# Kernel tuning notes

Measured on AMD Instinct MI355X. Metric: run time of the kernel, lower is better.

Reference implementation:

```python
import jax, jax.numpy as jnp
import numpy as np

B, L, XS, YS, A, C, NL = 32, 4096, 256, 256, 4, 64, 5  # batch, seq, x_size, y_size, n_actions, hid_cnn, cnn_layers


def _conv2d(x, w):
    # x: [N,Cin,H,W], w: [Cout,Cin,3,3], stride 1, pad 1 ('SAME')
    return jax.lax.conv_general_dilated(x, w, (1, 1), 'SAME',
                                        dimension_numbers=('NCHW', 'OIHW', 'NCHW'))


def setup_inputs() -> dict:
    key = jax.random.key(0)
    ks = jax.random.split(key, 16)
    stdv = 1.0 / np.sqrt(XS)
    inp = {
        'x': jax.random.normal(ks[0], (B, L, XS), jnp.float32),
        'y': jax.random.normal(ks[1], (B, YS), jnp.float32),
        'x_mask': jax.random.randint(ks[2], (B, L), 0, 2) == 1,
        'actions': jax.random.randint(ks[3], (B,), 0, A),
        'weight': jax.random.uniform(ks[4], (YS, XS), jnp.float32, -stdv, stdv),
    }
    chans = [(1, C)] + [(C, C)] * (NL - 2) + [(C, 1)]
    for i, (ci, co) in enumerate(chans):
        bound = 1.0 / np.sqrt(ci * 9)
        inp[f'cw{i}'] = jax.random.uniform(ks[5 + 2 * i], (A, co, ci, 3, 3), jnp.float32, -bound, bound)
        inp[f'cb{i}'] = jax.random.uniform(ks[6 + 2 * i], (A, co), jnp.float32, -bound, bound)
    return inp


def reference(x, y, x_mask, actions, weight,
              cw0, cb0, cw1, cb1, cw2, cb2, cw3, cb3, cw4, cb4):
    img = weight[None, None]  # [1,1,YS,XS] -- weight matrix as a 1-channel image

    def per_action(w0, b0, w1, b1, w2, b2, w3, b3, w4, b4):
        out = img
        layers = ((w0, b0), (w1, b1), (w2, b2), (w3, b3), (w4, b4))
        for i, (w, b) in enumerate(layers):
            out = _conv2d(out, w) + b[None, :, None, None]
            if i < NL - 1:
                out = jax.nn.relu(out)
        return out[0, 0]  # [YS,XS]

    # all per-action conv stacks batched via vmap -> [A,YS,XS]
    W_a = jax.vmap(per_action)(cw0, cb0, cw1, cb1, cw2, cb2, cw3, cb3, cw4, cb4)
    # one-hot multiply + sum over actions == select the per-sample action matrix
    Wy = jnp.einsum('bh,bhx->bx', y, W_a[actions])          # [B,XS]
    xWy = jnp.einsum('blx,bx->bl', x, Wy)                   # [B,L]
    xWy = jnp.where(x_mask, -jnp.inf, xWy)
    return jax.nn.softmax(xWy, axis=-1)  # eval-mode output (training uses log_softmax)
```

## Files before the change

### kernel.cpp

```cpp
#include <hip/hip_runtime.h>
#include <cstdint>
#include <cstddef>

typedef __attribute__((ext_vector_type(8))) short bf16x8;
typedef __attribute__((ext_vector_type(4))) float f32x4;
typedef __attribute__((ext_vector_type(4))) int i32x4;

__device__ inline unsigned short cvt_bf16_rne(float f) {
    unsigned u = __builtin_bit_cast(unsigned, f);
    u = (u + 0x7FFFu + ((u >> 16) & 1u)) >> 16;
    return (unsigned short)u;
}
__device__ inline float bf16_to_f32(unsigned short s) {
    return __builtin_bit_cast(float, (unsigned)s << 16);
}

__global__ void detect_mask_kernel(const unsigned int* m, int* flag) {
    int i = blockIdx.x * blockDim.x + threadIdx.x;
    int f = 0;
    #pragma unroll
    for (int k = 0; k < 4; ++k) {
        unsigned int v = m[i * 4 + k];
        if (v == 0x3F800000u) f |= 2;
        else if (v > 1u) f |= 1;
    }
    if (f) atomicOr(flag, f);
}

__global__ void apack_all_kernel(const float* __restrict__ cw1,
                                 const float* __restrict__ cw2,
                                 const float* __restrict__ cw3,
                                 char* __restrict__ apack,
                                 int* __restrict__ flag) {
    int t = threadIdx.x;
    int tap = blockIdx.x, a = blockIdx.y, lz = blockIdx.z;
    if (tap == 0 && a == 0 && lz == 0 && t == 0) *flag = 0;
    const float* cw = (lz == 0) ? cw1 : (lz == 1 ? cw2 : cw3);
    char* outp = apack + (size_t)lz * 294912;
    int ks = t >> 8, mf = (t >> 6) & 3, lane = t & 63;
    int n = lane & 15, q = lane >> 4;
    int co = mf * 16 + n;
    int ci0 = ks * 32 + q * 8;
    unsigned d[4];
    #pragma unroll
    for (int jj = 0; jj < 4; ++jj) {
        unsigned short h0 = cvt_bf16_rne(cw[((size_t)(a * 64 + co) * 64 + ci0 + 2 * jj + 0) * 9 + tap]);
        unsigned short h1 = cvt_bf16_rne(cw[((size_t)(a * 64 + co) * 64 + ci0 + 2 * jj + 1) * 9 + tap]);
        d[jj] = (unsigned)h0 | ((unsigned)h1 << 16);
    }
    *(i32x4*)(outp + ((((size_t)(a * 9 + tap) * 2 + ks) * 4 + mf) * 1024 + lane * 16)) =
        *(i32x4*)d;
}

__device__ __forceinline__ void conv_mid_body(const i32x4* lds4,
                                              const char* __restrict__ apack_l,
                                              const float* __restrict__ cb,
                                              unsigned short* __restrict__ act_out,
                                              int a, int r0, int c0, int tid) {
    int lane = tid & 63, wv = tid >> 6;
    int n = lane & 15, q = lane >> 4;

    f32x4 acc[4][4];
    #pragma unroll
    for (int mf = 0; mf < 4; ++mf) {
        f32x4 bb = *(const f32x4*)(cb + a * 64 + mf * 16 + q * 4);
        #pragma unroll
        for (int nf = 0; nf < 4; ++nf) acc[mf][nf] = bb;
    }

    int base_nf[4];
    #pragma unroll
    for (int nf = 0; nf < 4; ++nf) {
        int orl = wv * 2 + (nf >> 1);
        int ocl = ((nf & 1) << 4) + n;
        base_nf[nf] = (orl * 34 + ocl) * 9 + q;
    }
    const char* ap = apack_l + (size_t)a * 9 * 8192 + lane * 16;

    #pragma unroll
    for (int tap = 0; tap < 9; ++tap) {
        const int ty = tap / 3, tx = tap - ty * 3;
        const int toff = (ty * 34 + tx) * 9;
        #pragma unroll
        for (int ks = 0; ks < 2; ++ks) {
            bf16x8 Af[4], Bf[4];
            #pragma unroll
            for (int mf = 0; mf < 4; ++mf)
                Af[mf] = __builtin_bit_cast(bf16x8,
                    *(const i32x4*)(ap + (((tap * 2 + ks) * 4 + mf) << 10)));
            #pragma unroll
            for (int nf = 0; nf < 4; ++nf)
                Bf[nf] = __builtin_bit_cast(bf16x8, lds4[base_nf[nf] + toff + ks * 4]);
            #pragma unroll
            for (int mf = 0; mf < 4; ++mf)
                #pragma unroll
                for (int nf = 0; nf < 4; ++nf)
                    acc[mf][nf] = __builtin_amdgcn_mfma_f32_16x16x32_bf16(
                        Af[mf], Bf[nf], acc[mf][nf], 0, 0, 0);
        }
    }

    #pragma unroll
    for (int nf = 0; nf < 4; ++nf) {
        int grow = r0 + wv * 2 + (nf >> 1);
        int gcol = c0 + ((nf & 1) << 4) + n;
        char* ob = (char*)act_out + (((size_t)(a << 16) + (grow << 8) + gcol) << 7) + q * 8;
        #pragma unroll
        for (int mf = 0; mf < 4; ++mf) {
            f32x4 v = acc[mf][nf];
            unsigned d0 = (unsigned)cvt_bf16_rne(fmaxf(v.x, 0.0f))
                        | ((unsigned)cvt_bf16_rne(fmaxf(v.y, 0.0f)) << 16);
            unsigned d1 = (unsigned)cvt_bf16_rne(fmaxf(v.z, 0.0f))
                        | ((unsigned)cvt_bf16_rne(fmaxf(v.w, 0.0f)) << 16);
            uint2 st; st.x = d0; st.y = d1;
            *(uint2*)(ob + mf * 32) = st;
        }
    }
}

__global__ __launch_bounds__(256, 3)
void conv_mid_mfma(const unsigned short* __restrict__ act_in,
                   const char* __restrict__ apack_l,
                   const float* __restrict__ cb,
                   unsigned short* __restrict__ act_out) {
    __shared__ i32x4 lds4[340 * 9];
    int tid = threadIdx.x;
    int a = blockIdx.z;
    int r0 = blockIdx.y * 8, c0 = blockIdx.x * 32;
    const char* actb = (const char*)act_in;

    for (int s = tid; s < 2720; s += 256) {
        int px = s >> 3, o = s & 7;
        int prow = px / 34, pcol = px - prow * 34;
        int grow = r0 - 1 + prow, gcol = c0 - 1 + pcol;
        i32x4 v = {0, 0, 0, 0};
        if ((unsigned)grow < 256u && (unsigned)gcol < 256u)
            v = *(const i32x4*)(actb + (((size_t)(a << 16) + (grow << 8) + gcol) << 7) + (o << 4));
        lds4[px * 9 + o] = v;
    }
    __syncthreads();
    conv_mid_body(lds4, apack_l, cb, act_out, a, r0, c0, tid);
}

__global__ __launch_bounds__(256, 3)
void conv_mid_fused0(const float* __restrict__ img,
                     const float* __restrict__ cw0,
                     const float* __restrict__ cb0,
                     const char* __restrict__ apack_l,
                     const float* __restrict__ cb,
                     unsigned short* __restrict__ act_out) {
    __shared__ i32x4 lds4[340 * 9];
    __shared__ float img_s[12 * 36];
    int tid = threadIdx.x;
    int a = blockIdx.z;
    int r0 = blockIdx.y * 8, c0 = blockIdx.x * 32;

    for (int s = tid; s < 432; s += 256) {
        int ir = s / 36, ic = s - ir * 36;
        int gr = r0 - 2 + ir, gc = c0 - 2 + ic;
        img_s[s] = ((unsigned)gr < 256u && (unsigned)gc < 256u) ? img[gr * 256 + gc] : 0.0f;
    }
    __syncthreads();

    int o = tid & 7;
    float wr[8][9], br[8];
    #pragma unroll
    for (int j = 0; j < 8; ++j) {
        const float* wp = cw0 + ((size_t)a * 64 + o * 8 + j) * 9;
        #pragma unroll
        for (int t = 0; t < 9; ++t) wr[j][t] = wp[t];
        br[j] = cb0[a * 64 + o * 8 + j];
    }

    for (int s = tid; s < 2720; s += 256) {
        int px = s >> 3;
        int prow = px / 34, pcol = px - prow * 34;
        int grow = r0 - 1 + prow, gcol = c0 - 1 + pcol;
        i32x4 v = {0, 0, 0, 0};
        if ((unsigned)grow < 256u && (unsigned)gcol < 256u) {
            float accv[8];
            #pragma unroll
            for (int j = 0; j < 8; ++j) accv[j] = br[j];
            #pragma unroll
            for (int dy = 0; dy < 3; ++dy)
                #pragma unroll
                for (int dx = 0; dx < 3; ++dx) {
                    float iv = img_s[(prow + dy) * 36 + (pcol + dx)];
                    #pragma unroll
                    for (int j = 0; j < 8; ++j)
                        accv[j] = fmaf(wr[j][dy * 3 + dx], iv, accv[j]);
                }
            unsigned d[4];
            #pragma unroll
            for (int jj = 0; jj < 4; ++jj) {
                unsigned short h0 = cvt_bf16_rne(fmaxf(accv[2 * jj + 0], 0.0f));
                unsigned short h1 = cvt_bf16_rne(fmaxf(accv[2 * jj + 1], 0.0f));
                d[jj] = (unsigned)h0 | ((unsigned)h1 << 16);
            }
            v = *(i32x4*)d;
        }
        lds4[px * 9 + o] = v;
    }
    __syncthreads();
    conv_mid_body(lds4, apack_l, cb, act_out, a, r0, c0, tid);
}

__global__ void conv_last_kernel(const unsigned short* __restrict__ act,
                                 const float* __restrict__ cw4,
                                 const float* __restrict__ cb4,
                                 float* __restrict__ W_a) {
    int y = blockIdx.x, a = blockIdx.y;
    int tid = threadIdx.x;
    int lane = tid & 63, wv = tid >> 6;
    int o = lane & 7, pl = lane >> 3;
    float wr[8][9];
    #pragma unroll
    for (int j = 0; j < 8; ++j) {
        const float* wp = cw4 + ((size_t)a * 64 + o * 8 + j) * 9;
        #pragma unroll
        for (int t = 0; t < 9; ++t) wr[j][t] = wp[t];
    }
    const char* actb = (const char*)act;
    float bias = cb4[a];
    for (int i = 0; i < 8; ++i) {
        int x = i * 32 + wv * 8 + pl;
        float p = 0.0f;
        #pragma unroll
        for (int ty = 0; ty < 3; ++ty) {
            int py = y + ty - 1;
            #pragma unroll
            for (int tx = 0; tx < 3; ++tx) {
                int px = x + tx - 1;
                if ((unsigned)py < 256u && (unsigned)px < 256u) {
                    i32x4 v = *(const i32x4*)(actb +
                        (((size_t)(a << 16) + (py << 8) + px) << 7) + (o << 4));
                    const unsigned* dv = (const unsigned*)&v;
                    #pragma unroll
                    for (int j = 0; j < 8; ++j) {
                        unsigned d = dv[j >> 1];
                        unsigned short us = (j & 1) ? (unsigned short)(d >> 16)
                                                    : (unsigned short)(d & 0xffffu);
                        p = fmaf(bf16_to_f32(us), wr[j][ty * 3 + tx], p);
                    }
                }
            }
        }
        p += __shfl_xor(p, 1, 64);
        p += __shfl_xor(p, 2, 64);
        p += __shfl_xor(p, 4, 64);
        if (o == 0) W_a[(size_t)(a << 16) + (y << 8) + x] = p + bias;
    }
}

__global__ void wy_kernel(const float* __restrict__ yv,
                          const int* __restrict__ actions,
                          const float* __restrict__ W_a,
                          float* __restrict__ Wy) {
    int b = blockIdx.x, t = threadIdx.x;
    int x = t >> 2, hq = t & 3;
    int a = actions[b];
    const float* Wp = W_a + (size_t)a * 65536;
    const float* yb = yv + b * 256;
    float acc = 0.0f;
    #pragma unroll 8
    for (int i = 0; i < 64; ++i) {
        int h = i * 4 + hq;
        acc = fmaf(yb[h], Wp[(size_t)h * 256 + x], acc);
    }
    acc += __shfl_xor(acc, 1, 64);
    acc += __shfl_xor(acc, 2, 64);
    if (hq == 0) Wy[b * 256 + x] = acc;
}

__global__ __launch_bounds__(256)
void logits_kernel(const float* __restrict__ xv,
                   const void* __restrict__ mask,
                   const int* __restrict__ flag,
                   const float* __restrict__ Wy,
                   float* __restrict__ out) {
    int tid = threadIdx.x, lane = tid & 63, w = tid >> 6;
    int i = lane & 15, r = lane >> 4;
    int b = blockIdx.y;
    int fl = *flag;
    float4 wyv[4];
    #pragma unroll
    for (int k = 0; k < 4; ++k)
        wyv[k] = *(const float4*)(Wy + b * 256 + k * 64 + i * 4);
    const float* xb = xv + (size_t)b * 4096 * 256;
    float ninf = -__builtin_inff();
    int base0 = blockIdx.x * 64 + w * 16;

    #pragma unroll 1
    for (int it = 0; it < 4; ++it) {
        int row = base0 + it * 4 + r;
        const float* rp = xb + (size_t)row * 256 + i * 4;
        float4 xq[4];
        #pragma unroll
        for (int k = 0; k < 4; ++k)
            xq[k] = *(const float4*)(rp + k * 64);
        float p = 0.0f;
        #pragma unroll
        for (int k = 0; k < 4; ++k) {
            p = fmaf(xq[k].x, wyv[k].x, p);
            p = fmaf(xq[k].y, wyv[k].y, p);
            p = fmaf(xq[k].z, wyv[k].z, p);
            p = fmaf(xq[k].w, wyv[k].w, p);
        }
        p += __shfl_xor(p, 8, 64);
        p += __shfl_xor(p, 4, 64);
        p += __shfl_xor(p, 2, 64);
        p += __shfl_xor(p, 1, 64);
        if (i == 0) {
            size_t mi = (size_t)b * 4096 + row;
            bool msk;
            if (fl & 2)      msk = ((const float*)mask)[mi] != 0.0f;
            else if (fl & 1) msk = ((const unsigned char*)mask)[mi] != 0;
            else             msk = ((const int*)mask)[mi] != 0;
            out[mi] = msk ? ninf : p;
        }
    }
}

__global__ void softmax_kernel(float* __restrict__ out) {
    int b = blockIdx.x, tid = threadIdx.x;
    int lane = tid & 63, wid = tid >> 6;
    float* row = out + (size_t)b * 4096;
    float v[4];
    float m = -__builtin_inff();
    #pragma unroll
    for (int i = 0; i < 4; ++i) { v[i] = row[tid + i * 1024]; m = fmaxf(m, v[i]); }
    #pragma unroll
    for (int off = 32; off > 0; off >>= 1) m = fmaxf(m, __shfl_xor(m, off, 64));
    __shared__ float redm[16];
    __shared__ float reds[16];
    if (lane == 0) redm[wid] = m;
    __syncthreads();
    float M = redm[0];
    #pragma unroll
    for (int j = 1; j < 16; ++j) M = fmaxf(M, redm[j]);
    float s = 0.0f;
    #pragma unroll
    for (int i = 0; i < 4; ++i) { v[i] = expf(v[i] - M); s += v[i]; }
    #pragma unroll
    for (int off = 32; off > 0; off >>= 1) s += __shfl_xor(s, off, 64);
    if (lane == 0) reds[wid] = s;
    __syncthreads();
    float S = 0.0f;
    #pragma unroll
    for (int j = 0; j < 16; ++j) S += reds[j];
    float inv = 1.0f / S;
    #pragma unroll
    for (int i = 0; i < 4; ++i) row[tid + i * 1024] = v[i] * inv;
}

extern "C" void kernel_launch(void* const* d_in, const int* in_sizes, int n_in,
                              void* d_out, int out_size, void* d_ws, size_t ws_size,
                              hipStream_t stream) {
    const float* xv      = (const float*)d_in[0];
    const float* yv      = (const float*)d_in[1];
    const void*  xmask   = d_in[2];
    const int*   actions = (const int*)d_in[3];
    const float* weight  = (const float*)d_in[4];
    const float* cw0 = (const float*)d_in[5];
    const float* cb0 = (const float*)d_in[6];
    const float* cw1 = (const float*)d_in[7];
    const float* cb1 = (const float*)d_in[8];
    const float* cw2 = (const float*)d_in[9];
    const float* cb2 = (const float*)d_in[10];
    const float* cw3 = (const float*)d_in[11];
    const float* cb3 = (const float*)d_in[12];
    const float* cw4 = (const float*)d_in[13];
    const float* cb4 = (const float*)d_in[14];
    float* out = (float*)d_out;

    char* ws = (char*)d_ws;
    unsigned short* bufA = (unsigned short*)ws;
    unsigned short* bufB = (unsigned short*)(ws + 33554432);
    char*  apack = ws + 67108864;
    float* W_a   = (float*)(ws + 67993600);
    float* Wy    = (float*)(ws + 69042176);
    int*   flag  = (int*)(ws + 69074944);

    apack_all_kernel<<<dim3(9, 4, 3), 512, 0, stream>>>(cw1, cw2, cw3, apack, flag);
    detect_mask_kernel<<<32, 256, 0, stream>>>((const unsigned int*)xmask, flag);

    conv_mid_fused0<<<dim3(8, 32, 4), 256, 0, stream>>>(weight, cw0, cb0, apack, cb1, bufA);
    conv_mid_mfma<<<dim3(8, 32, 4), 256, 0, stream>>>(bufA, apack + 294912, cb2, bufB);
    conv_mid_mfma<<<dim3(8, 32, 4), 256, 0, stream>>>(bufB, apack + 589824, cb3, bufA);
    conv_last_kernel<<<dim3(256, 4), 256, 0, stream>>>(bufA, cw4, cb4, W_a);

    wy_kernel<<<32, 1024, 0, stream>>>(yv, actions, W_a, Wy);
    logits_kernel<<<dim3(64, 32), 256, 0, stream>>>(xv, xmask, flag, Wy, out);
    softmax_kernel<<<32, 1024, 0, stream>>>(out);
}
```

Measured before the change: 358.4 us.

## Fuse final 64-to-1 conv into layer-3 MFMA kernel via scatter atomics

The last conv layer (64 to 1 channel) now runs in the epilogue of the layer-3 MFMA kernel. Each pixel's ReLU'd, bf16-rounded activations are dotted with all 9 taps of cw4 and scattered into W_a with atomicAdd. This removes the bf16 activation write and reread plus a separate kernel launch. In exchange, W_a must be zeroed in the packing kernel and the cb4 bias is folded into wy_kernel as cb4*sum(y). Float atomic ordering makes the results nondeterministic.

Result: slower. 387.7 us (+8.2%).

```diff
diff --git a/kernel.cpp b/kernel.cpp
--- a/kernel.cpp
+++ b/kernel.cpp
@@ -30,11 +30,21 @@
 __global__ void apack_all_kernel(const float* __restrict__ cw1,
                                  const float* __restrict__ cw2,
                                  const float* __restrict__ cw3,
+                                 const float* __restrict__ cw4,
                                  char* __restrict__ apack,
+                                 float* __restrict__ W_a,
+                                 float* __restrict__ w4pack,
                                  int* __restrict__ flag) {
     int t = threadIdx.x;
     int tap = blockIdx.x, a = blockIdx.y, lz = blockIdx.z;
     if (tap == 0 && a == 0 && lz == 0 && t == 0) *flag = 0;
+
+    int gid = ((lz * 4 + a) * 9 + tap) * 512 + t;
+    for (int i = gid; i < 262144; i += 55296) W_a[i] = 0.0f;
+
+    if (lz == 0 && t < 64)
+        w4pack[(a * 9 + tap) * 64 + t] = cw4[(size_t)a * 576 + t * 9 + tap];
+
     const float* cw = (lz == 0) ? cw1 : (lz == 1 ? cw2 : cw3);
     char* outp = apack + (size_t)lz * 294912;
     int ks = t >> 8, mf = (t >> 6) & 3, lane = t & 63;
@@ -52,15 +62,14 @@
         *(i32x4*)d;
 }
 
-__device__ __forceinline__ void conv_mid_body(const i32x4* lds4,
-                                              const char* __restrict__ apack_l,
-                                              const float* __restrict__ cb,
-                                              unsigned short* __restrict__ act_out,
-                                              int a, int r0, int c0, int tid) {
+__device__ __forceinline__ void conv_mid_mainloop(const i32x4* lds4,
+                                                  const char* __restrict__ apack_l,
+                                                  const float* __restrict__ cb,
+                                                  f32x4 acc[4][4],
+                                                  int a, int tid) {
     int lane = tid & 63, wv = tid >> 6;
     int n = lane & 15, q = lane >> 4;
 
-    f32x4 acc[4][4];
     #pragma unroll
     for (int mf = 0; mf < 4; ++mf) {
         f32x4 bb = *(const f32x4*)(cb + a * 64 + mf * 16 + q * 4);
@@ -99,7 +108,13 @@
                         Af[mf], Bf[nf], acc[mf][nf], 0, 0, 0);
         }
     }
-
+}
+
+__device__ __forceinline__ void conv_mid_store(f32x4 acc[4][4],
+                                               unsigned short* __restrict__ act_out,
+                                               int a, int r0, int c0, int tid) {
+    int lane = tid & 63, wv = tid >> 6;
+    int n = lane & 15, q = lane >> 4;
     #pragma unroll
     for (int nf = 0; nf < 4; ++nf) {
         int grow = r0 + wv * 2 + (nf >> 1);
@@ -115,6 +130,20 @@
             uint2 st; st.x = d0; st.y = d1;
             *(uint2*)(ob + mf * 32) = st;
         }
+    }
+}
+
+__device__ __forceinline__ void conv_mid_stage(i32x4* lds4,
+                                               const char* __restrict__ actb,
+                                               int a, int r0, int c0, int tid) {
+    for (int s = tid; s < 2720; s += 256) {
+        int px = s >> 3, o = s & 7;
+        int prow = px / 34, pcol = px - prow * 34;
+        int grow = r0 - 1 + prow, gcol = c0 - 1 + pcol;
+        i32x4 v = {0, 0, 0, 0};
+        if ((unsigned)grow < 256u && (unsigned)gcol < 256u)
+            v = *(const i32x4*)(actb + (((size_t)(a << 16) + (grow << 8) + gcol) << 7) + (o << 4));
+        lds4[px * 9 + o] = v;
     }
 }
 
@@ -127,19 +156,80 @@
     int tid = threadIdx.x;
     int a = blockIdx.z;
     int r0 = blockIdx.y * 8, c0 = blockIdx.x * 32;
-    const char* actb = (const char*)act_in;
-
-    for (int s = tid; s < 2720; s += 256) {
-        int px = s >> 3, o = s & 7;
-        int prow = px / 34, pcol = px - prow * 34;
-        int grow = r0 - 1 + prow, gcol = c0 - 1 + pcol;
-        i32x4 v = {0, 0, 0, 0};
-        if ((unsigned)grow < 256u && (unsigned)gcol < 256u)
-            v = *(const i32x4*)(actb + (((size_t)(a << 16) + (grow << 8) + gcol) << 7) + (o << 4));
-        lds4[px * 9 + o] = v;
-    }
-    __syncthreads();
-    conv_mid_body(lds4, apack_l, cb, act_out, a, r0, c0, tid);
+    conv_mid_stage(lds4, (const char*)act_in, a, r0, c0, tid);
+    __syncthreads();
+    f32x4 acc[4][4];
+    conv_mid_mainloop(lds4, apack_l, cb, acc, a, tid);
+    conv_mid_store(acc, act_out, a, r0, c0, tid);
+}
+
+__global__ __launch_bounds__(256, 3)
+void conv_mid_last_fused(const unsigned short* __restrict__ act_in,
+                         const char* __restrict__ apack_l,
+                         const float* __restrict__ cb,
+                         const float* __restrict__ w4pack,
+                         float* __restrict__ W_a) {
+    __shared__ i32x4 lds4[340 * 9];
+    int tid = threadIdx.x;
+    int a = blockIdx.z;
+    int r0 = blockIdx.y * 8, c0 = blockIdx.x * 32;
+    conv_mid_stage(lds4, (const char*)act_in, a, r0, c0, tid);
+    __syncthreads();
+    f32x4 acc[4][4];
+    conv_mid_mainloop(lds4, apack_l, cb, acc, a, tid);
+
+    int lane = tid & 63, wv = tid >> 6;
+    int n = lane & 15, q = lane >> 4;
+    const float* w4p = w4pack + a * 576;
+
+    float part[4][9];
+    #pragma unroll
+    for (int nf = 0; nf < 4; ++nf)
+        #pragma unroll
+        for (int tap = 0; tap < 9; ++tap) part[nf][tap] = 0.0f;
+
+    #pragma unroll
+    for (int mf = 0; mf < 4; ++mf) {
+        f32x4 wq[9];
+        #pragma unroll
+        for (int tap = 0; tap < 9; ++tap)
+            wq[tap] = *(const f32x4*)(w4p + tap * 64 + mf * 16 + q * 4);
+        #pragma unroll
+        for (int nf = 0; nf < 4; ++nf) {
+            f32x4 v = acc[mf][nf];
+            float a0 = bf16_to_f32(cvt_bf16_rne(fmaxf(v.x, 0.0f)));
+            float a1 = bf16_to_f32(cvt_bf16_rne(fmaxf(v.y, 0.0f)));
+            float a2 = bf16_to_f32(cvt_bf16_rne(fmaxf(v.z, 0.0f)));
+            float a3 = bf16_to_f32(cvt_bf16_rne(fmaxf(v.w, 0.0f)));
+            #pragma unroll
+            for (int tap = 0; tap < 9; ++tap) {
+                float s = part[nf][tap];
+                s = fmaf(a0, wq[tap].x, s);
+                s = fmaf(a1, wq[tap].y, s);
+                s = fmaf(a2, wq[tap].z, s);
+                s = fmaf(a3, wq[tap].w, s);
+                part[nf][tap] = s;
+            }
+        }
+    }
+
+    #pragma unroll
+    for (int nf = 0; nf < 4; ++nf) {
+        int r = r0 + wv * 2 + (nf >> 1);
+        int c = c0 + ((nf & 1) << 4) + n;
+        #pragma unroll
+        for (int tap = 0; tap < 9; ++tap) {
+            float s = part[nf][tap];
+            s += __shfl_xor(s, 16, 64);
+            s += __shfl_xor(s, 32, 64);
+            if (q == 0) {
+                int ty = tap / 3, tx = tap - ty * 3;
+                int yy = r + 1 - ty, xx = c + 1 - tx;
+                if ((unsigned)yy < 256u && (unsigned)xx < 256u)
+                    atomicAdd(W_a + ((size_t)(a << 16) + (yy << 8) + xx), s);
+            }
+        }
+    }
 }
 
 __global__ __launch_bounds__(256, 3)
@@ -202,74 +292,34 @@
         lds4[px * 9 + o] = v;
     }
     __syncthreads();
-    conv_mid_body(lds4, apack_l, cb, act_out, a, r0, c0, tid);
-}
-
-__global__ void conv_last_kernel(const unsigned short* __restrict__ act,
-                                 const float* __restrict__ cw4,
-                                 const float* __restrict__ cb4,
-                                 float* __restrict__ W_a) {
-    int y = blockIdx.x, a = blockIdx.y;
-    int tid = threadIdx.x;
-    int lane = tid & 63, wv = tid >> 6;
-    int o = lane & 7, pl = lane >> 3;
-    float wr[8][9];
-    #pragma unroll
-    for (int j = 0; j < 8; ++j) {
-        const float* wp = cw4 + ((size_t)a * 64 + o * 8 + j) * 9;
-        #pragma unroll
-        for (int t = 0; t < 9; ++t) wr[j][t] = wp[t];
-    }
-    const char* actb = (const char*)act;
-    float bias = cb4[a];
-    for (int i = 0; i < 8; ++i) {
-        int x = i * 32 + wv * 8 + pl;
-        float p = 0.0f;
-        #pragma unroll
-        for (int ty = 0; ty < 3; ++ty) {
-            int py = y + ty - 1;
-            #pragma unroll
-            for (int tx = 0; tx < 3; ++tx) {
-                int px = x + tx - 1;
-                if ((unsigned)py < 256u && (unsigned)px < 256u) {
-                    i32x4 v = *(const i32x4*)(actb +
-                        (((size_t)(a << 16) + (py << 8) + px) << 7) + (o << 4));
-                    const unsigned* dv = (const unsigned*)&v;
-                    #pragma unroll
-                    for (int j = 0; j < 8; ++j) {
-                        unsigned d = dv[j >> 1];
-                        unsigned short us = (j & 1) ? (unsigned short)(d >> 16)
-                                                    : (unsigned short)(d & 0xffffu);
-                        p = fmaf(bf16_to_f32(us), wr[j][ty * 3 + tx], p);
-                    }
-                }
-            }
-        }
-        p += __shfl_xor(p, 1, 64);
-        p += __shfl_xor(p, 2, 64);
-        p += __shfl_xor(p, 4, 64);
-        if (o == 0) W_a[(size_t)(a << 16) + (y << 8) + x] = p + bias;
-    }
+    f32x4 acc[4][4];
+    conv_mid_mainloop(lds4, apack_l, cb, acc, a, tid);
+    conv_mid_store(acc, act_out, a, r0, c0, tid);
 }
 
 __global__ void wy_kernel(const float* __restrict__ yv,
                           const int* __restrict__ actions,
                           const float* __restrict__ W_a,
+                          const float* __restrict__ cb4,
                           float* __restrict__ Wy) {
     int b = blockIdx.x, t = threadIdx.x;
     int x = t >> 2, hq = t & 3;
     int a = actions[b];
     const float* Wp = W_a + (size_t)a * 65536;
     const float* yb = yv + b * 256;
-    float acc = 0.0f;
+    float acc = 0.0f, ys = 0.0f;
     #pragma unroll 8
     for (int i = 0; i < 64; ++i) {
         int h = i * 4 + hq;
-        acc = fmaf(yb[h], Wp[(size_t)h * 256 + x], acc);
+        float yh = yb[h];
+        ys += yh;
+        acc = fmaf(yh, Wp[(size_t)h * 256 + x], acc);
     }
     acc += __shfl_xor(acc, 1, 64);
     acc += __shfl_xor(acc, 2, 64);
-    if (hq == 0) Wy[b * 256 + x] = acc;
+    ys  += __shfl_xor(ys, 1, 64);
+    ys  += __shfl_xor(ys, 2, 64);
+    if (hq == 0) Wy[b * 256 + x] = acc + cb4[a] * ys;
 }
 
 __global__ __launch_bounds__(256)
@@ -376,20 +426,22 @@
     char* ws = (char*)d_ws;
     unsigned short* bufA = (unsigned short*)ws;
     unsigned short* bufB = (unsigned short*)(ws + 33554432);
-    char*  apack = ws + 67108864;
-    float* W_a   = (float*)(ws + 67993600);
-    float* Wy    = (float*)(ws + 69042176);
-    int*   flag  = (int*)(ws + 69074944);
-
-    apack_all_kernel<<<dim3(9, 4, 3), 512, 0, stream>>>(cw1, cw2, cw3, apack, flag);
+    char*  apack  = ws + 67108864;
+    float* W_a    = (float*)(ws + 67993600);
+    float* Wy     = (float*)(ws + 69042176);
+    int*   flag   = (int*)(ws + 69074944);
+    float* w4pack = (float*)(ws + 69075456);
+
+    apack_all_kernel<<<dim3(9, 4, 3), 512, 0, stream>>>(cw1, cw2, cw3, cw4,
+                                                        apack, W_a, w4pack, flag);
     detect_mask_kernel<<<32, 256, 0, stream>>>((const unsigned int*)xmask, flag);
 
     conv_mid_fused0<<<dim3(8, 32, 4), 256, 0, stream>>>(weight, cw0, cb0, apack, cb1, bufA);
     conv_mid_mfma<<<dim3(8, 32, 4), 256, 0, stream>>>(bufA, apack + 294912, cb2, bufB);
-    conv_mid_mfma<<<dim3(8, 32, 4), 256, 0, stream>>>(bufB, apack + 589824, cb3, bufA);
-    conv_last_kernel<<<dim3(256, 4), 256, 0, stream>>>(bufA, cw4, cb4, W_a);
-
-    wy_kernel<<<32, 1024, 0, stream>>>(yv, actions, W_a, Wy);
+    conv_mid_last_fused<<<dim3(8, 32, 4), 256, 0, stream>>>(bufB, apack + 589824, cb3,
+                                                            w4pack, W_a);
+
+    wy_kernel<<<32, 1024, 0, stream>>>(yv, actions, W_a, cb4, Wy);
     logits_kernel<<<dim3(64, 32), 256, 0, stream>>>(xv, xmask, flag, Wy, out);
     softmax_kernel<<<32, 1024, 0, stream>>>(out);
 }
```

## Tile last conv through LDS, fold mask detection into first conv, swizzle XCD

Applied to the files above, without the earlier changes.

The last conv layer is retiled into 8x32 spatial blocks that stage the bf16 activation halo in LDS, replacing per-pixel global loads that re-read each neighbour nine times. The separate mask-detection kernel is merged into the first conv launch as an extra z-slice of blocks, which saves one launch. Block indices are remapped with an XCD swizzle so neighbouring tiles of the same action run on the same chiplet and share L2. The changes add LDS pressure to the last conv kernel and a branch to the fused first kernel.

Result: faster. 341.6 us (-4.7%).

```diff
diff --git a/kernel.cpp b/kernel.cpp
--- a/kernel.cpp
+++ b/kernel.cpp
@@ -15,16 +15,8 @@
     return __builtin_bit_cast(float, (unsigned)s << 16);
 }
 
-__global__ void detect_mask_kernel(const unsigned int* m, int* flag) {
-    int i = blockIdx.x * blockDim.x + threadIdx.x;
-    int f = 0;
-    #pragma unroll
-    for (int k = 0; k < 4; ++k) {
-        unsigned int v = m[i * 4 + k];
-        if (v == 0x3F800000u) f |= 2;
-        else if (v > 1u) f |= 1;
-    }
-    if (f) atomicOr(flag, f);
+__device__ __forceinline__ int xcd_swz1024(int lin) {
+    return (lin & 7) * 128 + (lin >> 3);
 }
 
 __global__ void apack_all_kernel(const float* __restrict__ cw1,
@@ -52,15 +44,14 @@
         *(i32x4*)d;
 }
 
-__device__ __forceinline__ void conv_mid_body(const i32x4* lds4,
-                                              const char* __restrict__ apack_l,
-                                              const float* __restrict__ cb,
-                                              unsigned short* __restrict__ act_out,
-                                              int a, int r0, int c0, int tid) {
+__device__ __forceinline__ void conv_mid_mainloop(const i32x4* lds4,
+                                                  const char* __restrict__ apack_l,
+                                                  const float* __restrict__ cb,
+                                                  f32x4 acc[4][4],
+                                                  int a, int tid) {
     int lane = tid & 63, wv = tid >> 6;
     int n = lane & 15, q = lane >> 4;
 
-    f32x4 acc[4][4];
     #pragma unroll
     for (int mf = 0; mf < 4; ++mf) {
         f32x4 bb = *(const f32x4*)(cb + a * 64 + mf * 16 + q * 4);
@@ -99,7 +90,13 @@
                         Af[mf], Bf[nf], acc[mf][nf], 0, 0, 0);
         }
     }
-
+}
+
+__device__ __forceinline__ void conv_mid_store(f32x4 acc[4][4],
+                                               unsigned short* __restrict__ act_out,
+                                               int a, int r0, int c0, int tid) {
+    int lane = tid & 63, wv = tid >> 6;
+    int n = lane & 15, q = lane >> 4;
     #pragma unroll
     for (int nf = 0; nf < 4; ++nf) {
         int grow = r0 + wv * 2 + (nf >> 1);
@@ -118,17 +115,9 @@
     }
 }
 
-__global__ __launch_bounds__(256, 3)
-void conv_mid_mfma(const unsigned short* __restrict__ act_in,
-                   const char* __restrict__ apack_l,
-                   const float* __restrict__ cb,
-                   unsigned short* __restrict__ act_out) {
-    __shared__ i32x4 lds4[340 * 9];
-    int tid = threadIdx.x;
-    int a = blockIdx.z;
-    int r0 = blockIdx.y * 8, c0 = blockIdx.x * 32;
-    const char* actb = (const char*)act_in;
-
+__device__ __forceinline__ void conv_mid_stage(i32x4* lds4,
+                                               const char* __restrict__ actb,
+                                               int a, int r0, int c0, int tid) {
     for (int s = tid; s < 2720; s += 256) {
         int px = s >> 3, o = s & 7;
         int prow = px / 34, pcol = px - prow * 34;
@@ -138,8 +127,24 @@
             v = *(const i32x4*)(actb + (((size_t)(a << 16) + (grow << 8) + gcol) << 7) + (o << 4));
         lds4[px * 9 + o] = v;
     }
-    __syncthreads();
-    conv_mid_body(lds4, apack_l, cb, act_out, a, r0, c0, tid);
+}
+
+__global__ __launch_bounds__(256, 3)
+void conv_mid_mfma(const unsigned short* __restrict__ act_in,
+                   const char* __restrict__ apack_l,
+                   const float* __restrict__ cb,
+                   unsigned short* __restrict__ act_out) {
+    __shared__ i32x4 lds4[340 * 9];
+    int tid = threadIdx.x;
+    int lin = blockIdx.x + (blockIdx.y << 3) + (blockIdx.z << 8);
+    int wg = xcd_swz1024(lin);
+    int a = wg >> 8;
+    int r0 = ((wg >> 3) & 31) * 8, c0 = (wg & 7) * 32;
+    conv_mid_stage(lds4, (const char*)act_in, a, r0, c0, tid);
+    __syncthreads();
+    f32x4 acc[4][4];
+    conv_mid_mainloop(lds4, apack_l, cb, acc, a, tid);
+    conv_mid_store(acc, act_out, a, r0, c0, tid);
 }
 
 __global__ __launch_bounds__(256, 3)
@@ -148,12 +153,32 @@
                      const float* __restrict__ cb0,
                      const char* __restrict__ apack_l,
                      const float* __restrict__ cb,
-                     unsigned short* __restrict__ act_out) {
+                     unsigned short* __restrict__ act_out,
+                     const unsigned int* __restrict__ mask_u32,
+                     int* __restrict__ flag) {
     __shared__ i32x4 lds4[340 * 9];
     __shared__ float img_s[12 * 36];
     int tid = threadIdx.x;
-    int a = blockIdx.z;
-    int r0 = blockIdx.y * 8, c0 = blockIdx.x * 32;
+
+    if (blockIdx.z == 4) {
+        if (blockIdx.y < 4) {
+            int i = ((blockIdx.y * 8 + blockIdx.x) * 256 + tid);
+            int f = 0;
+            #pragma unroll
+            for (int k = 0; k < 4; ++k) {
+                unsigned int v = mask_u32[i * 4 + k];
+                if (v == 0x3F800000u) f |= 2;
+                else if (v > 1u) f |= 1;
+            }
+            if (f) atomicOr(flag, f);
+        }
+        return;
+    }
+
+    int lin = blockIdx.x + (blockIdx.y << 3) + (blockIdx.z << 8);
+    int wg = xcd_swz1024(lin);
+    int a = wg >> 8;
+    int r0 = ((wg >> 3) & 31) * 8, c0 = (wg & 7) * 32;
 
     for (int s = tid; s < 432; s += 256) {
         int ir = s / 36, ic = s - ir * 36;
@@ -202,15 +227,24 @@
         lds4[px * 9 + o] = v;
     }
     __syncthreads();
-    conv_mid_body(lds4, apack_l, cb, act_out, a, r0, c0, tid);
-}
-
-__global__ void conv_last_kernel(const unsigned short* __restrict__ act,
-                                 const float* __restrict__ cw4,
-                                 const float* __restrict__ cb4,
-                                 float* __restrict__ W_a) {
-    int y = blockIdx.x, a = blockIdx.y;
+    f32x4 acc[4][4];
+    conv_mid_mainloop(lds4, apack_l, cb, acc, a, tid);
+    conv_mid_store(acc, act_out, a, r0, c0, tid);
+}
+
+__global__ __launch_bounds__(256, 3)
+void conv_last_kernel(const unsigned short* __restrict__ act,
+                      const float* __restrict__ cw4,
+                      const float* __restrict__ cb4,
+                      float* __restrict__ W_a) {
+    __shared__ i32x4 lds4[340 * 9];
     int tid = threadIdx.x;
+    int lin = blockIdx.x + (blockIdx.y << 3) + (blockIdx.z << 8);
+    int wg = xcd_swz1024(lin);
+    int a = wg >> 8;
+    int r0 = ((wg >> 3) & 31) * 8, c0 = (wg & 7) * 32;
+    conv_mid_stage(lds4, (const char*)act, a, r0, c0, tid);
+
     int lane = tid & 63, wv = tid >> 6;
     int o = lane & 7, pl = lane >> 3;
     float wr[8][9];
@@ -220,35 +254,32 @@
         #pragma unroll
         for (int t = 0; t < 9; ++t) wr[j][t] = wp[t];
     }
-    const char* actb = (const char*)act;
     float bias = cb4[a];
-    for (int i = 0; i < 8; ++i) {
-        int x = i * 32 + wv * 8 + pl;
+    __syncthreads();
+
+    int c = wv * 8 + pl;
+    #pragma unroll 2
+    for (int r = 0; r < 8; ++r) {
         float p = 0.0f;
         #pragma unroll
-        for (int ty = 0; ty < 3; ++ty) {
-            int py = y + ty - 1;
+        for (int ty = 0; ty < 3; ++ty)
             #pragma unroll
             for (int tx = 0; tx < 3; ++tx) {
-                int px = x + tx - 1;
-                if ((unsigned)py < 256u && (unsigned)px < 256u) {
-                    i32x4 v = *(const i32x4*)(actb +
-                        (((size_t)(a << 16) + (py << 8) + px) << 7) + (o << 4));
-                    const unsigned* dv = (const unsigned*)&v;
-                    #pragma unroll
-                    for (int j = 0; j < 8; ++j) {
-                        unsigned d = dv[j >> 1];
-                        unsigned short us = (j & 1) ? (unsigned short)(d >> 16)
-                                                    : (unsigned short)(d & 0xffffu);
-                        p = fmaf(bf16_to_f32(us), wr[j][ty * 3 + tx], p);
-                    }
+                i32x4 v = lds4[((r + ty) * 34 + (c + tx)) * 9 + o];
+                const unsigned* dv = (const unsigned*)&v;
+                #pragma unroll
+                for (int j = 0; j < 8; ++j) {
+                    unsigned d = dv[j >> 1];
+                    unsigned short us = (j & 1) ? (unsigned short)(d >> 16)
+                                                : (unsigned short)(d & 0xffffu);
+                    p = fmaf(bf16_to_f32(us), wr[j][ty * 3 + tx], p);
                 }
             }
-        }
         p += __shfl_xor(p, 1, 64);
         p += __shfl_xor(p, 2, 64);
         p += __shfl_xor(p, 4, 64);
-        if (o == 0) W_a[(size_t)(a << 16) + (y << 8) + x] = p + bias;
+        if (o == 0)
+            W_a[(size_t)(a << 16) + ((r0 + r) << 8) + (c0 + c)] = p + bias;
     }
 }
 
@@ -382,12 +413,12 @@
     int*   flag  = (int*)(ws + 69074944);
 
     apack_all_kernel<<<dim3(9, 4, 3), 512, 0, stream>>>(cw1, cw2, cw3, apack, flag);
-    detect_mask_kernel<<<32, 256, 0, stream>>>((const unsigned int*)xmask, flag);
-
-    conv_mid_fused0<<<dim3(8, 32, 4), 256, 0, stream>>>(weight, cw0, cb0, apack, cb1, bufA);
+
+    conv_mid_fused0<<<dim3(8, 32, 5), 256, 0, stream>>>(weight, cw0, cb0, apack, cb1, bufA,
+                                                        (const unsigned int*)xmask, flag);
     conv_mid_mfma<<<dim3(8, 32, 4), 256, 0, stream>>>(bufA, apack + 294912, cb2, bufB);
     conv_mid_mfma<<<dim3(8, 32, 4), 256, 0, stream>>>(bufB, apack + 589824, cb3, bufA);
-    conv_last_kernel<<<dim3(256, 4), 256, 0, stream>>>(bufA, cw4, cb4, W_a);
+    conv_last_kernel<<<dim3(8, 32, 4), 256, 0, stream>>>(bufA, cw4, cb4, W_a);
 
     wy_kernel<<<32, 1024, 0, stream>>>(yv, actions, W_a, Wy);
     logits_kernel<<<dim3(64, 32), 256, 0, stream>>>(xv, xmask, flag, Wy, out);
```
